# Kernel tuning notes

Measured on AMD Instinct MI355X. Metric: run time of the kernel, lower is better.

The kernel has to match this reference:

```python
import jax, jax.numpy as jnp
import numpy as np

G = 256          # grid resolution -> V = G*G vertices
B = 8            # batch of meshes
N_SAMPLES = 2048
W_CHAMFER, W_EDGE, W_NORMAL, W_LAP = 1.0, 1.0, 0.1, 0.1
V = G * G


def _grid_faces(g):
    idx = np.arange(g * g).reshape(g, g)
    v00 = idx[:-1, :-1].ravel(); v01 = idx[:-1, 1:].ravel()
    v10 = idx[1:, :-1].ravel();  v11 = idx[1:, 1:].ravel()
    f1 = np.stack([v00, v01, v10], 1)
    f2 = np.stack([v01, v11, v10], 1)
    return np.concatenate([f1, f2], 0).astype(np.int32)  # [F,3]


def _edges_and_pairs(faces, n_verts):
    # all face-edge incidences + the opposite vertex of each incidence
    e = np.concatenate([faces[:, [0, 1]], faces[:, [1, 2]], faces[:, [0, 2]]], 0)
    opp = np.concatenate([faces[:, 2], faces[:, 0], faces[:, 1]], 0)
    e = np.sort(e, 1)
    key = e[:, 0].astype(np.int64) * n_verts + e[:, 1]
    order = np.argsort(key, kind='stable')
    key_s, es, opps = key[order], e[order], opp[order]
    first = np.ones(len(key_s), bool); first[1:] = key_s[1:] != key_s[:-1]
    edges = es[first].astype(np.int32)                      # unique undirected edges [E,2]
    dup = np.nonzero(~first)[0]                             # 2nd incidence of shared edges
    pairs = np.stack([es[dup - 1, 0], es[dup - 1, 1], opps[dup - 1], opps[dup]], 1).astype(np.int32)  # [P,4]
    return edges, pairs


def setup_inputs() -> dict:
    key = jax.random.key(0)
    faces = _grid_faces(G)
    edges, nc_pairs = _edges_and_pairs(faces, V)
    # base grid geometry + gaussian perturbation (realistic smooth-ish surfaces)
    xs, ys = np.meshgrid(np.linspace(0, 1, G), np.linspace(0, 1, G), indexing='ij')
    base = np.stack([xs, ys, 0.1 * np.sin(4 * np.pi * xs) * np.cos(4 * np.pi * ys)], -1).reshape(V, 3)
    k1, k2 = jax.random.split(key)
    verts_pred = jnp.asarray(base, jnp.float32)[None] + 0.01 * jax.random.normal(k1, (B, V, 3), jnp.float32)
    verts_targ = jnp.asarray(base, jnp.float32)[None] + 0.01 * jax.random.normal(k2, (B, V, 3), jnp.float32)
    return {
        'verts_pred': verts_pred,
        'verts_targ': verts_targ,
        'faces': jnp.asarray(faces),
        'edges': jnp.asarray(edges),
        'nc_pairs': jnp.asarray(nc_pairs),
    }


def _sample_points(verts, faces, key, n):
    # verts [V,3]; area-weighted face sampling + uniform barycentric (pytorch3d scheme)
    v0, v1, v2 = verts[faces[:, 0]], verts[faces[:, 1]], verts[faces[:, 2]]
    areas = 0.5 * jnp.linalg.norm(jnp.cross(v1 - v0, v2 - v0), axis=-1)          # [F]
    kf, kb = jax.random.split(key)
    fidx = jax.random.categorical(kf, jnp.log(areas + 1e-12), shape=(n,))        # [n]
    uv = jax.random.uniform(kb, (n, 2), verts.dtype)
    su = jnp.sqrt(uv[:, 0:1]); vv = uv[:, 1:2]
    w0, w1, w2 = 1.0 - su, su * (1.0 - vv), su * vv
    return w0 * v0[fidx] + w1 * v1[fidx] + w2 * v2[fidx]                         # [n,3]


def _chamfer(x, y):
    # squared-distance chamfer, mean over points then batch, both directions summed
    d = jnp.sum((x[:, :, None, :] - y[:, None, :, :]) ** 2, -1)                  # [B,N,M]
    return jnp.mean(jnp.min(d, axis=2)) + jnp.mean(jnp.min(d, axis=1))


def _edge_loss(verts, edges):
    diff = verts[:, edges[:, 0]] - verts[:, edges[:, 1]]                          # [B,E,3]
    return jnp.mean(jnp.sum(diff * diff, -1))                                     # (||e|| - 0)^2


def _normal_consistency(verts, nc_pairs):
    v0 = verts[:, nc_pairs[:, 0]]; v1 = verts[:, nc_pairs[:, 1]]
    a = verts[:, nc_pairs[:, 2]]; b = verts[:, nc_pairs[:, 3]]
    e = v1 - v0
    n0 = jnp.cross(e, a - v0)
    n1 = -jnp.cross(e, b - v0)
    eps = 1e-8
    cos = jnp.sum(n0 * n1, -1) / (
        jnp.maximum(jnp.linalg.norm(n0, axis=-1), eps)
        * jnp.maximum(jnp.linalg.norm(n1, axis=-1), eps))
    return jnp.mean(1.0 - cos)


def _laplacian_uniform(verts, edges):
    e0, e1 = edges[:, 0], edges[:, 1]
    ones = jnp.ones((edges.shape[0],), verts.dtype)

    def per_mesh(v):  # v [V,3]
        nsum = (jax.ops.segment_sum(v[e1], e0, num_segments=V)
                + jax.ops.segment_sum(v[e0], e1, num_segments=V))
        deg = (jax.ops.segment_sum(ones, e0, num_segments=V)
               + jax.ops.segment_sum(ones, e1, num_segments=V))
        lap = nsum / jnp.maximum(deg, 1.0)[:, None] - v                           # D^-1 A v - v
        return jnp.mean(jnp.linalg.norm(lap, axis=-1))

    return jnp.mean(jax.vmap(per_mesh)(verts))


def reference(verts_pred, verts_targ, faces, edges, nc_pairs):
    skey = jax.random.key(42)
    kp = jax.random.split(jax.random.fold_in(skey, 0), verts_pred.shape[0])
    kt = jax.random.split(jax.random.fold_in(skey, 1), verts_targ.shape[0])
    sample_pred = jax.vmap(lambda v, k: _sample_points(v, faces, k, N_SAMPLES))(verts_pred, kp)
    sample_targ = jax.vmap(lambda v, k: _sample_points(v, faces, k, N_SAMPLES))(verts_targ, kt)
    loss_chamfer = _chamfer(sample_pred, sample_targ)
    loss_edge = _edge_loss(verts_pred, edges)
    loss_normal = _normal_consistency(verts_pred, nc_pairs)
    loss_lap = _laplacian_uniform(verts_pred, edges)
    loss = (W_CHAMFER * loss_chamfer + W_EDGE * loss_edge
            + W_NORMAL * loss_normal + W_LAP * loss_lap)
    return (loss, loss_chamfer, loss_edge, loss_normal, loss_lap)
```

## Files before the change

kernel.cpp:

```cpp
#include <hip/hip_runtime.h>
#include <stdint.h>

#define GSZ 256
#define NV (GSZ*GSZ)
#define NS 2048
#define CELLS (255*255)
#define FH CELLS
#define NF (2*CELLS)
#define CH 8

struct F3 { float x, y, z; };

__device__ __forceinline__ F3 ldv3(const float* __restrict__ p, int idx) {
    const float* q = p + 3*(size_t)idx;
    F3 r; r.x = q[0]; r.y = q[1]; r.z = q[2]; return r;
}
__device__ __forceinline__ F3 f3sub(F3 a, F3 b) { return F3{a.x-b.x, a.y-b.y, a.z-b.z}; }
__device__ __forceinline__ F3 f3cross(F3 a, F3 b) {
    return F3{a.y*b.z - a.z*b.y, a.z*b.x - a.x*b.z, a.x*b.y - a.y*b.x};
}
__device__ __forceinline__ float f3dot(F3 a, F3 b) { return a.x*b.x + a.y*b.y + a.z*b.z; }

__device__ __forceinline__ uint64_t splitmix64(uint64_t& s) {
    s += 0x9E3779B97F4A7C15ULL;
    uint64_t z = s;
    z = (z ^ (z >> 30)) * 0xBF58476D1CE4E5B9ULL;
    z = (z ^ (z >> 27)) * 0x94D049BB133111EBULL;
    return z ^ (z >> 31);
}

__device__ __forceinline__ float blockReduceSum256(float v) {
    __shared__ float s[4];
    int lane = threadIdx.x & 63, w = threadIdx.x >> 6;
    #pragma unroll
    for (int o = 32; o > 0; o >>= 1) v += __shfl_down(v, o, 64);
    if (lane == 0) s[w] = v;
    __syncthreads();
    if (threadIdx.x == 0) v = s[0] + s[1] + s[2] + s[3];
    return v;
}

__global__ void k_area(const float* __restrict__ vp, const float* __restrict__ vt,
                       int B, float* __restrict__ areas, float* __restrict__ blockmax) {
    int gid = blockIdx.x*256 + threadIdx.x;
    int total = 2*B*CELLS;
    float mloc = 0.f;
    if (gid < total) {
        int m = gid / CELLS;
        int c = gid - m*CELLS;
        int i = c / 255, j = c - i*255;
        const float* verts = (m < B ? vp + (size_t)m*NV*3
                                    : vt + (size_t)(m-B)*NV*3);
        int b00 = i*GSZ + j;
        F3 v00 = ldv3(verts, b00);
        F3 v01 = ldv3(verts, b00+1);
        F3 v10 = ldv3(verts, b00+GSZ);
        F3 v11 = ldv3(verts, b00+GSZ+1);
        F3 c1 = f3cross(f3sub(v01, v00), f3sub(v10, v00));
        F3 c2 = f3cross(f3sub(v11, v01), f3sub(v10, v01));
        float a1 = 0.5f * sqrtf(f3dot(c1, c1));
        float a2 = 0.5f * sqrtf(f3dot(c2, c2));
        size_t base = (size_t)m*NF;
        areas[base + c]      = a1;
        areas[base + FH + c] = a2;
        mloc = fmaxf(a1, a2);
    }
    #pragma unroll
    for (int o = 32; o > 0; o >>= 1) mloc = fmaxf(mloc, __shfl_down(mloc, o, 64));
    __shared__ float s[4];
    int lane = threadIdx.x & 63, w = threadIdx.x >> 6;
    if (lane == 0) s[w] = mloc;
    __syncthreads();
    if (threadIdx.x == 0)
        blockmax[blockIdx.x] = fmaxf(fmaxf(s[0], s[1]), fmaxf(s[2], s[3]));
}

__global__ void k_sample(const float* __restrict__ vp, const float* __restrict__ vt,
                         int B, const float* __restrict__ areas,
                         const float* __restrict__ blockmax, int nbm,
                         float* __restrict__ samples) {
    float m = 0.f;
    for (int k = threadIdx.x; k < nbm; k += 256) m = fmaxf(m, blockmax[k]);
    #pragma unroll
    for (int o = 32; o > 0; o >>= 1) m = fmaxf(m, __shfl_down(m, o, 64));
    __shared__ float s[4];
    int lane = threadIdx.x & 63, w = threadIdx.x >> 6;
    if (lane == 0) s[w] = m;
    __syncthreads();
    __shared__ float sMaxA;
    if (threadIdx.x == 0) sMaxA = fmaxf(fmaxf(s[0], s[1]), fmaxf(s[2], s[3]));
    __syncthreads();
    float maxA = sMaxA;

    int gid = blockIdx.x*256 + threadIdx.x;
    int cloud = gid / (B*NS);
    int rem = gid - cloud*(B*NS);
    int b = rem / NS;
    const float* verts = (cloud ? vt : vp) + (size_t)b*NV*3;
    const float* am = areas + (size_t)(cloud*B + b)*NF;

    uint64_t st = ((uint64_t)(gid + 1) * 0x9E3779B97F4A7C15ULL) ^ 0xC0FFEE123456789ULL;
    int f = 0;
    for (int round = 0; round < 64; ++round) {
        uint64_t r0 = splitmix64(st), r1 = splitmix64(st);
        uint64_t r2 = splitmix64(st), r3 = splitmix64(st);
        int f0 = (int)(((uint64_t)(uint32_t)r0 * (uint32_t)NF) >> 32);
        int f1 = (int)(((uint64_t)(uint32_t)r1 * (uint32_t)NF) >> 32);
        int f2 = (int)(((uint64_t)(uint32_t)r2 * (uint32_t)NF) >> 32);
        int f3 = (int)(((uint64_t)(uint32_t)r3 * (uint32_t)NF) >> 32);
        float a0 = am[f0], a1 = am[f1], a2 = am[f2], a3 = am[f3];
        float u0 = ((uint32_t)(r0 >> 40)) * (1.f/16777216.f);
        float u1 = ((uint32_t)(r1 >> 40)) * (1.f/16777216.f);
        float u2 = ((uint32_t)(r2 >> 40)) * (1.f/16777216.f);
        float u3 = ((uint32_t)(r3 >> 40)) * (1.f/16777216.f);
        if (u0 * maxA <= a0) { f = f0; break; }
        if (u1 * maxA <= a1) { f = f1; break; }
        if (u2 * maxA <= a2) { f = f2; break; }
        if (u3 * maxA <= a3) { f = f3; break; }
        f = f3;
    }
    int i0, i1, i2;
    if (f < FH) {
        int c = f;  int i = c / 255, j = c - i*255;  int v = i*GSZ + j;
        i0 = v; i1 = v + 1; i2 = v + GSZ;
    } else {
        int c = f - FH;  int i = c / 255, j = c - i*255;  int v = i*GSZ + j;
        i0 = v + 1; i1 = v + GSZ + 1; i2 = v + GSZ;
    }
    F3 v0 = ldv3(verts, i0), v1 = ldv3(verts, i1), v2 = ldv3(verts, i2);
    uint64_t r = splitmix64(st);
    float u0 = ((uint32_t)r >> 8) * (1.f/16777216.f);
    float u1 = ((uint32_t)(r >> 32) >> 8) * (1.f/16777216.f);
    float su = sqrtf(u0);
    float w0 = 1.f - su, w1 = su * (1.f - u1), w2 = su * u1;
    float* o = samples + (size_t)gid*3;
    o[0] = w0*v0.x + w1*v1.x + w2*v2.x;
    o[1] = w0*v0.y + w1*v1.y + w2*v2.y;
    o[2] = w0*v0.z + w1*v1.z + w2*v2.z;
}

__global__ void k_chamfer(const float* __restrict__ samples, int B,
                          float* __restrict__ minpart) {
    int dir = blockIdx.z >> 4, q = blockIdx.z & 15;
    int b = blockIdx.y, xh = blockIdx.x;
    const float* src = samples + ((size_t)dir*B + b)*NS*3;
    const float* dst = samples + ((size_t)(1-dir)*B + b)*NS*3;

    __shared__ float4 tile[128];
    if (threadIdx.x < 128) {
        const float* p = dst + (size_t)(q*128 + threadIdx.x)*3;
        tile[threadIdx.x] = make_float4(p[0], p[1], p[2], 0.f);
    }
    float px[4], py[4], pz[4], mn[4];
    #pragma unroll
    for (int k = 0; k < 4; ++k) {
        int i = xh*1024 + k*256 + threadIdx.x;
        const float* p = src + (size_t)i*3;
        px[k] = p[0]; py[k] = p[1]; pz[k] = p[2];
        mn[k] = 3.402823466e38f;
    }
    __syncthreads();
    #pragma unroll 2
    for (int j = 0; j < 128; ++j) {
        float4 t = tile[j];
        #pragma unroll
        for (int k = 0; k < 4; ++k) {
            float dx = px[k]-t.x, dy = py[k]-t.y, dz = pz[k]-t.z;
            mn[k] = fminf(mn[k], dx*dx + dy*dy + dz*dz);
        }
    }
    float* outp = minpart + (((size_t)(dir*B + b)*16) + q)*NS;
    #pragma unroll
    for (int k = 0; k < 4; ++k)
        outp[xh*1024 + k*256 + threadIdx.x] = mn[k];
}

__global__ void k_cham_reduce(const float* __restrict__ minpart, int B,
                              float* __restrict__ chamPart) {
    int gid = blockIdx.x*256 + threadIdx.x;
    int dir = gid / (B*NS);
    int rem = gid - dir*(B*NS);
    int b = rem / NS, i = rem - b*NS;
    const float* p = minpart + (size_t)(dir*B + b)*16*NS + i;
    float mn = 3.402823466e38f;
    #pragma unroll
    for (int q = 0; q < 16; ++q) mn = fminf(mn, p[(size_t)q*NS]);
    float sm = blockReduceSum256(mn);
    if (threadIdx.x == 0) chamPart[blockIdx.x] = sm;
}

__global__ void k_mesh(const float* __restrict__ vp, const int* __restrict__ edges,
                       const int* __restrict__ ncp, int B, int E, int P,
                       int nbE, int nbP,
                       float* __restrict__ partE, float* __restrict__ partP,
                       float* __restrict__ partV) {
    int bx = blockIdx.x, b = blockIdx.y;
    const float* verts = vp + (size_t)b*NV*3;
    float acc = 0.f;
    if (bx < nbE) {
        int base = bx*(256*CH);
        #pragma unroll 2
        for (int c = 0; c < CH; ++c) {
            int e = base + c*256 + threadIdx.x;
            if (e < E) {
                int2 ed = ((const int2*)edges)[e];
                F3 d = f3sub(ldv3(verts, ed.x), ldv3(verts, ed.y));
                acc += f3dot(d, d);
            }
        }
        float s = blockReduceSum256(acc);
        if (threadIdx.x == 0) partE[(size_t)bx*B + b] = s;
    } else if (bx < nbE + nbP) {
        int base = (bx - nbE)*(256*CH);
        for (int c = 0; c < CH; ++c) {
            int p = base + c*256 + threadIdx.x;
            if (p < P) {
                int4 q = ((const int4*)ncp)[p];
                F3 v0 = ldv3(verts, q.x), v1 = ldv3(verts, q.y);
                F3 a = ldv3(verts, q.z), bb = ldv3(verts, q.w);
                F3 e = f3sub(v1, v0);
                F3 n0 = f3cross(e, f3sub(a, v0));
                F3 n1 = f3cross(f3sub(bb, v0), e);
                float num = f3dot(n0, n1);
                float den = fmaxf(sqrtf(f3dot(n0, n0)), 1e-8f) *
                            fmaxf(sqrtf(f3dot(n1, n1)), 1e-8f);
                acc += 1.f - num / den;
            }
        }
        float s = blockReduceSum256(acc);
        if (threadIdx.x == 0) partP[(size_t)(bx - nbE)*B + b] = s;
    } else {
        int base = (bx - nbE - nbP)*(256*CH);
        for (int c = 0; c < CH; ++c) {
            int idx = base + c*256 + threadIdx.x;
            int i = idx >> 8, j = idx & 255;
            F3 ctr = ldv3(verts, idx);
            float nx = 0.f, ny = 0.f, nz = 0.f; int deg = 0;
            #define ADDN(ii, jj) { F3 n_ = ldv3(verts, (ii)*GSZ + (jj)); \
                                   nx += n_.x; ny += n_.y; nz += n_.z; ++deg; }
            if (j > 0)               ADDN(i, j-1);
            if (j < GSZ-1)           ADDN(i, j+1);
            if (i > 0)               ADDN(i-1, j);
            if (i < GSZ-1)           ADDN(i+1, j);
            if (i < GSZ-1 && j > 0)  ADDN(i+1, j-1);
            if (i > 0 && j < GSZ-1)  ADDN(i-1, j+1);
            #undef ADDN
            float inv = 1.f / (float)deg;
            float lx = nx*inv - ctr.x, ly = ny*inv - ctr.y, lz = nz*inv - ctr.z;
            acc += sqrtf(lx*lx + ly*ly + lz*lz);
        }
        float s = blockReduceSum256(acc);
        if (threadIdx.x == 0) partV[(size_t)(bx - nbE - nbP)*B + b] = s;
    }
}

__global__ void k_final(const float* __restrict__ chamPart,
                        const float* __restrict__ partE, int nE,
                        const float* __restrict__ partP, int nP,
                        const float* __restrict__ partV, int nL,
                        int B, int E, int P, float* __restrict__ out) {
    double a0 = 0, a1 = 0, aE = 0, aP = 0, aL = 0;
    for (int k = threadIdx.x; k < 64;  k += 256) a0 += (double)chamPart[k];
    for (int k = 64 + threadIdx.x; k < 128; k += 256) a1 += (double)chamPart[k];
    for (int k = threadIdx.x; k < nE; k += 256) aE += (double)partE[k];
    for (int k = threadIdx.x; k < nP; k += 256) aP += (double)partP[k];
    for (int k = threadIdx.x; k < nL; k += 256) aL += (double)partV[k];
    __shared__ double sd[5][4];
    double v[5] = {a0, a1, aE, aP, aL};
    int lane = threadIdx.x & 63, w = threadIdx.x >> 6;
    #pragma unroll
    for (int r = 0; r < 5; ++r) {
        double x = v[r];
        #pragma unroll
        for (int o = 32; o > 0; o >>= 1) x += __shfl_down(x, o, 64);
        if (lane == 0) sd[r][w] = x;
    }
    __syncthreads();
    if (threadIdx.x == 0) {
        double bn = (double)B * NS;
        double ch = (sd[0][0]+sd[0][1]+sd[0][2]+sd[0][3]) / bn
                  + (sd[1][0]+sd[1][1]+sd[1][2]+sd[1][3]) / bn;
        double ed = (sd[2][0]+sd[2][1]+sd[2][2]+sd[2][3]) / ((double)B * E);
        double no = (sd[3][0]+sd[3][1]+sd[3][2]+sd[3][3]) / ((double)B * P);
        double la = (sd[4][0]+sd[4][1]+sd[4][2]+sd[4][3]) / ((double)B * NV);
        double loss = ch + ed + 0.1*no + 0.1*la;
        out[0] = (float)loss; out[1] = (float)ch; out[2] = (float)ed;
        out[3] = (float)no;   out[4] = (float)la;
    }
}

extern "C" void kernel_launch(void* const* d_in, const int* in_sizes, int n_in,
                              void* d_out, int out_size, void* d_ws, size_t ws_size,
                              hipStream_t stream) {
    const float* vp = (const float*)d_in[0];
    const float* vt = (const float*)d_in[1];
    const int* edges = (const int*)d_in[3];
    const int* ncp   = (const int*)d_in[4];
    const int B = in_sizes[0] / (3*NV);
    const int E = in_sizes[3] / 2;
    const int P = in_sizes[4] / 4;

    char* ws = (char*)d_ws;
    size_t off = 0;
    float* areas    = (float*)(ws + off); off += (size_t)2*B*NF*sizeof(float);
    float* samples  = (float*)(ws + off); off += (size_t)2*B*NS*3*sizeof(float);
    float* minpart  = (float*)(ws + off); off += (size_t)2*B*16*NS*sizeof(float);
    float* blockmax = (float*)(ws + off); off += 8192*sizeof(float);
    float* chamPart = (float*)(ws + off); off += 256*sizeof(float);
    float* partE    = (float*)(ws + off); off += 2048*sizeof(float);
    float* partP    = (float*)(ws + off); off += 2048*sizeof(float);
    float* partV    = (float*)(ws + off); off += 1024*sizeof(float);

    int nbm = (2*B*CELLS + 255)/256;
    k_area<<<nbm, 256, 0, stream>>>(vp, vt, B, areas, blockmax);
    k_sample<<<(2*B*NS)/256, 256, 0, stream>>>(vp, vt, B, areas, blockmax, nbm, samples);
    dim3 gch(2, B, 32);
    k_chamfer<<<gch, 256, 0, stream>>>(samples, B, minpart);
    k_cham_reduce<<<(2*B*NS)/256, 256, 0, stream>>>(minpart, B, chamPart);
    int nbE = (E + 256*CH - 1)/(256*CH);
    int nbP = (P + 256*CH - 1)/(256*CH);
    int nbV = NV/(256*CH);
    dim3 gm(nbE + nbP + nbV, B);
    k_mesh<<<gm, 256, 0, stream>>>(vp, edges, ncp, B, E, P, nbE, nbP,
                                   partE, partP, partV);
    k_final<<<1, 256, 0, stream>>>(chamPart, partE, nbE*B, partP, nbP*B,
                                   partV, nbV*B, B, E, P, (float*)d_out);
}
```

Baseline: 147.3 us.

## Merge chamfer and mesh-loss kernels, fuse reduce+final via last-block ticket

```diff
diff --git a/kernel.cpp b/kernel.cpp
--- a/kernel.cpp
+++ b/kernel.cpp
@@ -41,7 +41,9 @@
 }
 
 __global__ void k_area(const float* __restrict__ vp, const float* __restrict__ vt,
-                       int B, float* __restrict__ areas, float* __restrict__ blockmax) {
+                       int B, float* __restrict__ areas, float* __restrict__ blockmax,
+                       unsigned* __restrict__ counter) {
+    if (blockIdx.x == 0 && threadIdx.x == 0) *counter = 0u;
     int gid = blockIdx.x*256 + threadIdx.x;
     int total = 2*B*CELLS;
     float mloc = 0.f;
@@ -78,7 +80,7 @@
 __global__ void k_sample(const float* __restrict__ vp, const float* __restrict__ vt,
                          int B, const float* __restrict__ areas,
                          const float* __restrict__ blockmax, int nbm,
-                         float* __restrict__ samples) {
+                         float4* __restrict__ samples) {
     float m = 0.f;
     for (int k = threadIdx.x; k < nbm; k += 256) m = fmaxf(m, blockmax[k]);
     #pragma unroll
@@ -133,72 +135,62 @@
     float u1 = ((uint32_t)(r >> 32) >> 8) * (1.f/16777216.f);
     float su = sqrtf(u0);
     float w0 = 1.f - su, w1 = su * (1.f - u1), w2 = su * u1;
-    float* o = samples + (size_t)gid*3;
-    o[0] = w0*v0.x + w1*v1.x + w2*v2.x;
-    o[1] = w0*v0.y + w1*v1.y + w2*v2.y;
-    o[2] = w0*v0.z + w1*v1.z + w2*v2.z;
-}
-
-__global__ void k_chamfer(const float* __restrict__ samples, int B,
-                          float* __restrict__ minpart) {
-    int dir = blockIdx.z >> 4, q = blockIdx.z & 15;
-    int b = blockIdx.y, xh = blockIdx.x;
-    const float* src = samples + ((size_t)dir*B + b)*NS*3;
-    const float* dst = samples + ((size_t)(1-dir)*B + b)*NS*3;
-
-    __shared__ float4 tile[128];
-    if (threadIdx.x < 128) {
-        const float* p = dst + (size_t)(q*128 + threadIdx.x)*3;
-        tile[threadIdx.x] = make_float4(p[0], p[1], p[2], 0.f);
-    }
-    float px[4], py[4], pz[4], mn[4];
-    #pragma unroll
-    for (int k = 0; k < 4; ++k) {
-        int i = xh*1024 + k*256 + threadIdx.x;
-        const float* p = src + (size_t)i*3;
-        px[k] = p[0]; py[k] = p[1]; pz[k] = p[2];
-        mn[k] = 3.402823466e38f;
-    }
-    __syncthreads();
-    #pragma unroll 2
-    for (int j = 0; j < 128; ++j) {
-        float4 t = tile[j];
+    float X = w0*v0.x + w1*v1.x + w2*v2.x;
+    float Y = w0*v0.y + w1*v1.y + w2*v2.y;
+    float Z = w0*v0.z + w1*v1.z + w2*v2.z;
+    samples[gid] = make_float4(X, Y, Z, X*X + Y*Y + Z*Z);
+}
+
+__global__ void k_heavy(const float* __restrict__ vp,
+                        const float4* __restrict__ samples,
+                        const int* __restrict__ edges, const int* __restrict__ ncp,
+                        int B, int E, int P, int nbE, int nbP,
+                        float* __restrict__ minpart,
+                        float* __restrict__ partE, float* __restrict__ partP,
+                        float* __restrict__ partV) {
+    int bx = blockIdx.x, b = blockIdx.y;
+    if (bx < 64) {
+        int xh = bx >> 5, z = bx & 31;
+        int dir = z >> 4, q = z & 15;
+        const float4* src = samples + ((size_t)dir*B + b)*NS;
+        const float4* dst = samples + ((size_t)(1-dir)*B + b)*NS;
+
+        __shared__ float4 tile[128];
+        if (threadIdx.x < 128) tile[threadIdx.x] = dst[q*128 + threadIdx.x];
+
+        float nx[4], ny[4], nz[4], xx[4], mn[4];
         #pragma unroll
         for (int k = 0; k < 4; ++k) {
-            float dx = px[k]-t.x, dy = py[k]-t.y, dz = pz[k]-t.z;
-            mn[k] = fminf(mn[k], dx*dx + dy*dy + dz*dz);
-        }
-    }
-    float* outp = minpart + (((size_t)(dir*B + b)*16) + q)*NS;
-    #pragma unroll
-    for (int k = 0; k < 4; ++k)
-        outp[xh*1024 + k*256 + threadIdx.x] = mn[k];
-}
-
-__global__ void k_cham_reduce(const float* __restrict__ minpart, int B,
-                              float* __restrict__ chamPart) {
-    int gid = blockIdx.x*256 + threadIdx.x;
-    int dir = gid / (B*NS);
-    int rem = gid - dir*(B*NS);
-    int b = rem / NS, i = rem - b*NS;
-    const float* p = minpart + (size_t)(dir*B + b)*16*NS + i;
-    float mn = 3.402823466e38f;
-    #pragma unroll
-    for (int q = 0; q < 16; ++q) mn = fminf(mn, p[(size_t)q*NS]);
-    float sm = blockReduceSum256(mn);
-    if (threadIdx.x == 0) chamPart[blockIdx.x] = sm;
-}
-
-__global__ void k_mesh(const float* __restrict__ vp, const int* __restrict__ edges,
-                       const int* __restrict__ ncp, int B, int E, int P,
-                       int nbE, int nbP,
-                       float* __restrict__ partE, float* __restrict__ partP,
-                       float* __restrict__ partV) {
-    int bx = blockIdx.x, b = blockIdx.y;
+            int i = xh*1024 + k*256 + threadIdx.x;
+            float4 sp = src[i];
+            nx[k] = -2.f*sp.x; ny[k] = -2.f*sp.y; nz[k] = -2.f*sp.z;
+            xx[k] = sp.w;
+            mn[k] = 3.402823466e38f;
+        }
+        __syncthreads();
+        #pragma unroll 4
+        for (int j = 0; j < 128; ++j) {
+            float4 t = tile[j];
+            #pragma unroll
+            for (int k = 0; k < 4; ++k) {
+                float d = fmaf(nx[k], t.x, t.w);
+                d = fmaf(ny[k], t.y, d);
+                d = fmaf(nz[k], t.z, d);
+                mn[k] = fminf(mn[k], d);
+            }
+        }
+        float* outp = minpart + (((size_t)(dir*B + b)*16) + q)*NS;
+        #pragma unroll
+        for (int k = 0; k < 4; ++k)
+            outp[xh*1024 + k*256 + threadIdx.x] = mn[k] + xx[k];
+        return;
+    }
+
+    int mx = bx - 64;
     const float* verts = vp + (size_t)b*NV*3;
     float acc = 0.f;
-    if (bx < nbE) {
-        int base = bx*(256*CH);
+    if (mx < nbE) {
+        int base = mx*(256*CH);
         #pragma unroll 2
         for (int c = 0; c < CH; ++c) {
             int e = base + c*256 + threadIdx.x;
@@ -209,9 +201,9 @@
             }
         }
         float s = blockReduceSum256(acc);
-        if (threadIdx.x == 0) partE[(size_t)bx*B + b] = s;
-    } else if (bx < nbE + nbP) {
-        int base = (bx - nbE)*(256*CH);
+        if (threadIdx.x == 0) partE[(size_t)mx*B + b] = s;
+    } else if (mx < nbE + nbP) {
+        int base = (mx - nbE)*(256*CH);
         for (int c = 0; c < CH; ++c) {
             int p = base + c*256 + threadIdx.x;
             if (p < P) {
@@ -222,15 +214,14 @@
                 F3 n0 = f3cross(e, f3sub(a, v0));
                 F3 n1 = f3cross(f3sub(bb, v0), e);
                 float num = f3dot(n0, n1);
-                float den = fmaxf(sqrtf(f3dot(n0, n0)), 1e-8f) *
-                            fmaxf(sqrtf(f3dot(n1, n1)), 1e-8f);
-                acc += 1.f - num / den;
+                float den2 = fmaxf(f3dot(n0, n0), 1e-16f) * fmaxf(f3dot(n1, n1), 1e-16f);
+                acc += 1.f - num * rsqrtf(den2);
             }
         }
         float s = blockReduceSum256(acc);
-        if (threadIdx.x == 0) partP[(size_t)(bx - nbE)*B + b] = s;
+        if (threadIdx.x == 0) partP[(size_t)(mx - nbE)*B + b] = s;
     } else {
-        int base = (bx - nbE - nbP)*(256*CH);
+        int base = (mx - nbE - nbP)*(256*CH);
         for (int c = 0; c < CH; ++c) {
             int idx = base + c*256 + threadIdx.x;
             int i = idx >> 8, j = idx & 255;
@@ -250,18 +241,42 @@
             acc += sqrtf(lx*lx + ly*ly + lz*lz);
         }
         float s = blockReduceSum256(acc);
-        if (threadIdx.x == 0) partV[(size_t)(bx - nbE - nbP)*B + b] = s;
-    }
-}
-
-__global__ void k_final(const float* __restrict__ chamPart,
-                        const float* __restrict__ partE, int nE,
-                        const float* __restrict__ partP, int nP,
-                        const float* __restrict__ partV, int nL,
-                        int B, int E, int P, float* __restrict__ out) {
+        if (threadIdx.x == 0) partV[(size_t)(mx - nbE - nbP)*B + b] = s;
+    }
+}
+
+__global__ void k_redfin(const float* __restrict__ minpart, int B,
+                         const float* __restrict__ partE, int nE,
+                         const float* __restrict__ partP, int nP,
+                         const float* __restrict__ partV, int nL,
+                         int E, int P,
+                         float* __restrict__ chamPart,
+                         unsigned* __restrict__ counter,
+                         float* __restrict__ out) {
+    int gid = blockIdx.x*256 + threadIdx.x;
+    int dir = gid / (B*NS);
+    int rem = gid - dir*(B*NS);
+    int b = rem / NS, i = rem - b*NS;
+    const float* p = minpart + (size_t)(dir*B + b)*16*NS + i;
+    float mn = 3.402823466e38f;
+    #pragma unroll
+    for (int q = 0; q < 16; ++q) mn = fminf(mn, p[(size_t)q*NS]);
+    float sm = blockReduceSum256(mn);
+    if (threadIdx.x == 0) chamPart[blockIdx.x] = sm;
+
+    __shared__ unsigned sTicket;
+    if (threadIdx.x == 0) {
+        __threadfence();
+        sTicket = atomicAdd(counter, 1u);
+    }
+    __syncthreads();
+    if (sTicket != (unsigned)(gridDim.x - 1)) return;
+    __threadfence();
+
+    const volatile float* cp = chamPart;
     double a0 = 0, a1 = 0, aE = 0, aP = 0, aL = 0;
-    for (int k = threadIdx.x; k < 64;  k += 256) a0 += (double)chamPart[k];
-    for (int k = 64 + threadIdx.x; k < 128; k += 256) a1 += (double)chamPart[k];
+    for (int k = threadIdx.x; k < 64;  k += 256) a0 += (double)cp[k];
+    for (int k = 64 + threadIdx.x; k < 128; k += 256) a1 += (double)cp[k];
     for (int k = threadIdx.x; k < nE; k += 256) aE += (double)partE[k];
     for (int k = threadIdx.x; k < nP; k += 256) aP += (double)partP[k];
     for (int k = threadIdx.x; k < nL; k += 256) aL += (double)partV[k];
@@ -302,27 +317,32 @@
 
     char* ws = (char*)d_ws;
     size_t off = 0;
-    float* areas    = (float*)(ws + off); off += (size_t)2*B*NF*sizeof(float);
-    float* samples  = (float*)(ws + off); off += (size_t)2*B*NS*3*sizeof(float);
-    float* minpart  = (float*)(ws + off); off += (size_t)2*B*16*NS*sizeof(float);
-    float* blockmax = (float*)(ws + off); off += 8192*sizeof(float);
-    float* chamPart = (float*)(ws + off); off += 256*sizeof(float);
-    float* partE    = (float*)(ws + off); off += 2048*sizeof(float);
-    float* partP    = (float*)(ws + off); off += 2048*sizeof(float);
-    float* partV    = (float*)(ws + off); off += 1024*sizeof(float);
+    auto alloc = [&](size_t bytes) -> void* {
+        void* p = ws + off;
+        off = (off + bytes + 255) & ~(size_t)255;
+        return p;
+    };
+    float*    areas    = (float*)   alloc((size_t)2*B*NF*sizeof(float));
+    float4*   samples  = (float4*)  alloc((size_t)2*B*NS*sizeof(float4));
+    float*    minpart  = (float*)   alloc((size_t)2*B*16*NS*sizeof(float));
+    float*    blockmax = (float*)   alloc(8192*sizeof(float));
+    float*    chamPart = (float*)   alloc(256*sizeof(float));
+    float*    partE    = (float*)   alloc(2048*sizeof(float));
+    float*    partP    = (float*)   alloc(2048*sizeof(float));
+    float*    partV    = (float*)   alloc(1024*sizeof(float));
+    unsigned* counter  = (unsigned*)alloc(256);
 
     int nbm = (2*B*CELLS + 255)/256;
-    k_area<<<nbm, 256, 0, stream>>>(vp, vt, B, areas, blockmax);
+    k_area<<<nbm, 256, 0, stream>>>(vp, vt, B, areas, blockmax, counter);
     k_sample<<<(2*B*NS)/256, 256, 0, stream>>>(vp, vt, B, areas, blockmax, nbm, samples);
-    dim3 gch(2, B, 32);
-    k_chamfer<<<gch, 256, 0, stream>>>(samples, B, minpart);
-    k_cham_reduce<<<(2*B*NS)/256, 256, 0, stream>>>(minpart, B, chamPart);
     int nbE = (E + 256*CH - 1)/(256*CH);
     int nbP = (P + 256*CH - 1)/(256*CH);
     int nbV = NV/(256*CH);
-    dim3 gm(nbE + nbP + nbV, B);
-    k_mesh<<<gm, 256, 0, stream>>>(vp, edges, ncp, B, E, P, nbE, nbP,
-                                   partE, partP, partV);
-    k_final<<<1, 256, 0, stream>>>(chamPart, partE, nbE*B, partP, nbP*B,
-                                   partV, nbV*B, B, E, P, (float*)d_out);
-}
+    dim3 gh(64 + nbE + nbP + nbV, B);
+    k_heavy<<<gh, 256, 0, stream>>>(vp, samples, edges, ncp, B, E, P, nbE, nbP,
+                                    minpart, partE, partP, partV);
+    k_redfin<<<(2*B*NS)/256, 256, 0, stream>>>(minpart, B, partE, nbE*B,
+                                               partP, nbP*B, partV, nbV*B,
+                                               E, P, chamPart, counter,
+                                               (float*)d_out);
+}
```

New measurement: 144.1 us (median of 2 runs). 1.02x faster.
